# Kernel tuning notes

Hardware: AMD Instinct MI355X
Metric: run time of the kernel (lower is better)

## Reference

```python
import jax, jax.numpy as jnp
import numpy as np


def setup_inputs() -> dict:
    key = jax.random.key(0)
    ks = jax.random.split(key, 8)
    B, S, Nc, C, Cseed = 4, 4096, 8192, 512, 256
    return {
        "query_xyz": jax.random.normal(ks[0], (B, S, 3), dtype=jnp.float32),
        "ref_xyz": jax.random.normal(ks[1], (B, Nc, 3), dtype=jnp.float32),
        "ref_feat": jax.random.normal(ks[2], (B, C, Nc), dtype=jnp.float32),
        "seed_features": jax.random.normal(ks[3], (B, Cseed, S), dtype=jnp.float32),
        "W_seed_proj": jax.random.normal(ks[4], (Cseed, C), dtype=jnp.float32) * 0.02,
        "b_seed_proj": jax.random.normal(ks[5], (Cseed,), dtype=jnp.float32) * 0.02,
        "W_concat_proj": jax.random.normal(ks[6], (Cseed, 2 * Cseed), dtype=jnp.float32) * 0.02,
        "b_concat_proj": jax.random.normal(ks[7], (Cseed,), dtype=jnp.float32) * 0.02,
    }


def _nn_gather(query_xyz, ref_xyz, ref_feat):
    # torch.cdist(p=2) + argmin: argmin over squared distance is identical
    # (sqrt is monotonic), so we skip the sqrt.
    q2 = jnp.sum(query_xyz * query_xyz, axis=-1, keepdims=True)      # (B,S,1)
    r2 = jnp.sum(ref_xyz * ref_xyz, axis=-1)[:, None, :]             # (B,1,Nc)
    qr = jnp.einsum("bsd,bnd->bsn", query_xyz, ref_xyz)              # (B,S,Nc)
    d2 = q2 + r2 - 2.0 * qr                                          # (B,S,Nc)
    idx = jnp.argmin(d2, axis=-1)                                    # (B,S) int
    # gather nearest-neighbor features: (B,C,Nc) -> (B,C,S)
    return jnp.take_along_axis(ref_feat, idx[:, None, :], axis=2)


def reference(query_xyz, ref_xyz, ref_feat, seed_features,
              W_seed_proj, b_seed_proj, W_concat_proj, b_concat_proj):
    lift3d_raw = _nn_gather(query_xyz, ref_xyz, ref_feat)            # (B,C,S)
    # 1x1 Conv1d == channel matmul
    lift3d_seed = jnp.einsum("oc,bcs->bos", W_seed_proj, lift3d_raw) \
                  + b_seed_proj[None, :, None]                       # (B,256,S)
    fused = jnp.concatenate([seed_features, lift3d_seed], axis=1)    # (B,512,S)
    out = jnp.einsum("oc,bcs->bos", W_concat_proj, fused) \
          + b_concat_proj[None, :, None]                             # (B,256,S)
    return out
```

## Files before the change

kernel.cpp:

```cpp
#include <hip/hip_runtime.h>

#define B_   4
#define S_   4096
#define NC   8192
#define C_   512
#define CS   256
#define KTOT 768

typedef __attribute__((ext_vector_type(8))) short short8;
typedef __attribute__((ext_vector_type(4))) float f32x4;

static __device__ __forceinline__ unsigned short f2bf(float x) {
    unsigned u = __builtin_bit_cast(unsigned, x);
    unsigned r = u + 0x7FFFu + ((u >> 16) & 1u);
    return (unsigned short)(r >> 16);
}

__global__ __launch_bounds__(256) void prep_kernel(
        const float* __restrict__ rxyz, float4* __restrict__ refpk,
        const float* __restrict__ Wcat, const float* __restrict__ Wseed,
        unsigned short* __restrict__ Wcomb,
        const float* __restrict__ bseed, const float* __restrict__ bcat,
        float* __restrict__ beff,
        const float* __restrict__ seed, unsigned short* __restrict__ seedT) {
    __shared__ float sa[64][68];
    __shared__ float sbt[64][68];
    int bid = blockIdx.x;
    int tid = threadIdx.x;

    if (bid < 64) {
        int w = tid >> 6, l = tid & 63;
        int o = bid * 4 + w;
        float4 wv = *(const float4*)(Wcat + (size_t)o * 512 + 256 + l * 4);
        float4 bb = *(const float4*)(bseed + l * 4);
        float acc = __fmul_rn(wv.x, bb.x);
        acc = fmaf(wv.y, bb.y, acc);
        acc = fmaf(wv.z, bb.z, acc);
        acc = fmaf(wv.w, bb.w, acc);
        #pragma unroll
        for (int off = 32; off > 0; off >>= 1) acc += __shfl_down(acc, off);
        if (l == 0) beff[o] = acc + bcat[o];
    } else if (bid < 96) {
        int xb = bid - 64;
        int tc = (xb & 7) * 64;
        int to = (xb >> 3) * 64;
        int tx = tid & 15, ty = tid >> 4;
        float acc[4][4] = {};
        for (int kt = 0; kt < 256; kt += 64) {
            __syncthreads();
            #pragma unroll
            for (int r = 0; r < 4; ++r) {
                int oo = r * 16 + ty;
                float4 v = *(const float4*)(Wcat + (size_t)(to + oo) * 512 + 256 + kt + tx * 4);
                sa[oo][tx * 4 + 0] = v.x;
                sa[oo][tx * 4 + 1] = v.y;
                sa[oo][tx * 4 + 2] = v.z;
                sa[oo][tx * 4 + 3] = v.w;
                float4 u = *(const float4*)(Wseed + (size_t)(kt + oo) * 512 + tc + tx * 4);
                sbt[oo][tx * 4 + 0] = u.x;
                sbt[oo][tx * 4 + 1] = u.y;
                sbt[oo][tx * 4 + 2] = u.z;
                sbt[oo][tx * 4 + 3] = u.w;
            }
            __syncthreads();
            for (int k = 0; k < 64; ++k) {
                float a[4], bb2[4];
                #pragma unroll
                for (int i = 0; i < 4; ++i) a[i] = sa[ty * 4 + i][k];
                #pragma unroll
                for (int j = 0; j < 4; ++j) bb2[j] = sbt[k][tx * 4 + j];
                #pragma unroll
                for (int i = 0; i < 4; ++i)
                    #pragma unroll
                    for (int j = 0; j < 4; ++j)
                        acc[i][j] = fmaf(a[i], bb2[j], acc[i][j]);
            }
        }
        #pragma unroll
        for (int i = 0; i < 4; ++i)
            #pragma unroll
            for (int j = 0; j < 4; ++j)
                Wcomb[(size_t)(to + ty * 4 + i) * KTOT + 256 + tc + tx * 4 + j] = f2bf(acc[i][j]);
    } else if (bid < 160) {
        int g = ((bid - 96) * 256 + tid) * 4;
        int o = g >> 8, cc = g & 255;
        float4 v = *(const float4*)(Wcat + (size_t)o * 512 + cc);
        ushort4 ov;
        ov.x = f2bf(v.x); ov.y = f2bf(v.y); ov.z = f2bf(v.z); ov.w = f2bf(v.w);
        *(ushort4*)(Wcomb + (size_t)o * KTOT + cc) = ov;
    } else if (bid < 288) {
        int gid = (bid - 160) * 256 + tid;
        float x = rxyz[gid * 3 + 0];
        float y = rxyz[gid * 3 + 1];
        float z = rxyz[gid * 3 + 2];
        float r2 = __fadd_rn(__fadd_rn(__fmul_rn(x, x), __fmul_rn(y, y)), __fmul_rn(z, z));
        refpk[gid] = make_float4(x, y, z, r2);
    } else {
        int id = bid - 288;
        int b = id >> 8;
        int rem = id & 255;
        int c0 = (rem >> 6) * 64;
        int s0 = (rem & 63) * 64;
        int tx = tid & 15, ty = tid >> 4;
        #pragma unroll
        for (int r = 0; r < 4; ++r) {
            int cc = r * 16 + ty;
            float4 v = *(const float4*)(seed + ((size_t)b * CS + c0 + cc) * S_ + s0 + tx * 4);
            sa[tx * 4 + 0][cc] = v.x;
            sa[tx * 4 + 1][cc] = v.y;
            sa[tx * 4 + 2][cc] = v.z;
            sa[tx * 4 + 3][cc] = v.w;
        }
        __syncthreads();
        #pragma unroll
        for (int r = 0; r < 4; ++r) {
            int n = r * 16 + ty;
            ushort4 o;
            o.x = f2bf(sa[n][tx * 4 + 0]);
            o.y = f2bf(sa[n][tx * 4 + 1]);
            o.z = f2bf(sa[n][tx * 4 + 2]);
            o.w = f2bf(sa[n][tx * 4 + 3]);
            *(ushort4*)(seedT + ((size_t)b * S_ + s0 + n) * CS + c0 + tx * 4) = o;
        }
    }
}

__global__ __launch_bounds__(256, 4) void mid_kernel(
        const float* __restrict__ qxyz, const float4* __restrict__ refpk,
        float* __restrict__ pval, int* __restrict__ pidx,
        const float* __restrict__ rf, unsigned short* __restrict__ refT) {
    __shared__ float t[64][65];
    int bid = blockIdx.x;
    int tid = threadIdx.x;

    if (bid % 3 != 0) {
        int id = bid - bid / 3 - 1;
        int b = id >> 10;
        int c0 = ((id >> 7) & 7) * 64;
        int n0 = (id & 127) * 64;
        int tx = tid & 15, ty = tid >> 4;
        #pragma unroll
        for (int r = 0; r < 4; ++r) {
            int cc = r * 16 + ty;
            float4 v = *(const float4*)(rf + ((size_t)b * C_ + c0 + cc) * NC + n0 + tx * 4);
            t[tx * 4 + 0][cc] = v.x;
            t[tx * 4 + 1][cc] = v.y;
            t[tx * 4 + 2][cc] = v.z;
            t[tx * 4 + 3][cc] = v.w;
        }
        __syncthreads();
        #pragma unroll
        for (int r = 0; r < 4; ++r) {
            int n = r * 16 + ty;
            ushort4 o;
            o.x = f2bf(t[n][tx * 4 + 0]);
            o.y = f2bf(t[n][tx * 4 + 1]);
            o.z = f2bf(t[n][tx * 4 + 2]);
            o.w = f2bf(t[n][tx * 4 + 3]);
            *(ushort4*)(refT + ((size_t)b * NC + n0 + n) * C_ + c0 + tx * 4) = o;
        }
    } else {
        int aid = bid / 3;
        int sblk = aid & 127;
        int c = (aid >> 7) & 3;
        int b = aid >> 9;
        int lane = tid & 63;
        int qg = tid >> 6;
        int sbase = sblk * 32 + qg * 8;

        float qx[8], qy[8], qz[8], q2[8];
        #pragma unroll
        for (int q = 0; q < 8; ++q) {
            const float* qp = qxyz + ((size_t)(b * S_ + sbase + q)) * 3;
            qx[q] = qp[0]; qy[q] = qp[1]; qz[q] = qp[2];
            q2[q] = __fadd_rn(__fadd_rn(__fmul_rn(qx[q], qx[q]), __fmul_rn(qy[q], qy[q])),
                              __fmul_rn(qz[q], qz[q]));
        }

        const float4* ep = refpk + (size_t)b * NC + c * 2048 + lane;
        float best[8];
        int bj[8];
        #pragma unroll
        for (int q = 0; q < 8; ++q) { best[q] = 3.4028235e38f; bj[q] = 0; }

        float4 r0 = ep[0];
        float4 r1 = ep[64];
        #pragma unroll 2
        for (int j = 0; j < 32; j += 2) {
            float4 r2 = r0, r3 = r1;
            if (j + 2 < 32) {
                r2 = ep[(j + 2) * 64];
                r3 = ep[(j + 3) * 64];
            }
            #pragma unroll
            for (int q = 0; q < 8; ++q) {
                float qr = __fadd_rn(__fadd_rn(__fmul_rn(qx[q], r0.x), __fmul_rn(qy[q], r0.y)),
                                     __fmul_rn(qz[q], r0.z));
                float s = __fadd_rn(q2[q], r0.w);
                float d2 = fmaf(qr, -2.0f, s);
                if (d2 < best[q]) { best[q] = d2; bj[q] = j; }
            }
            #pragma unroll
            for (int q = 0; q < 8; ++q) {
                float qr = __fadd_rn(__fadd_rn(__fmul_rn(qx[q], r1.x), __fmul_rn(qy[q], r1.y)),
                                     __fmul_rn(qz[q], r1.z));
                float s = __fadd_rn(q2[q], r1.w);
                float d2 = fmaf(qr, -2.0f, s);
                if (d2 < best[q]) { best[q] = d2; bj[q] = j + 1; }
            }
            r0 = r2;
            r1 = r3;
        }

        int bx[8];
        #pragma unroll
        for (int q = 0; q < 8; ++q) bx[q] = c * 2048 + bj[q] * 64 + lane;

        #pragma unroll
        for (int m = 1; m < 64; m <<= 1) {
            #pragma unroll
            for (int q = 0; q < 8; ++q) {
                float vv = __shfl_xor(best[q], m, 64);
                int xx = __shfl_xor(bx[q], m, 64);
                if (vv < best[q] || (vv == best[q] && xx < bx[q])) {
                    best[q] = vv; bx[q] = xx;
                }
            }
        }
        if (lane == 0) {
            #pragma unroll
            for (int q = 0; q < 8; ++q) {
                int qs = b * S_ + sbase + q;
                pval[qs * 4 + c] = best[q];
                pidx[qs * 4 + c] = bx[q];
            }
        }
    }
}

__global__ __launch_bounds__(256) void fused_gemm_kernel(
        const unsigned short* __restrict__ Wcomb,
        const unsigned short* __restrict__ seedT,
        const unsigned short* __restrict__ refT,
        const float* __restrict__ pval,
        const int* __restrict__ pidx,
        const float* __restrict__ beff,
        float* __restrict__ out) {
    __shared__ __align__(16) unsigned short sA[64][72];
    __shared__ __align__(16) unsigned short sB[64][72];
    __shared__ int sIdx[64];
    __shared__ float sBias[64];

    int tid = threadIdx.x;
    int b = blockIdx.z;
    int m0 = blockIdx.y * 64;
    int s0 = blockIdx.x * 64;
    if (tid < 64) {
        int qs = b * S_ + s0 + tid;
        float v = pval[qs * 4 + 0];
        int x = pidx[qs * 4 + 0];
        #pragma unroll
        for (int c = 1; c < 4; ++c) {
            float vv = pval[qs * 4 + c];
            int xx = pidx[qs * 4 + c];
            if (vv < v || (vv == v && xx < x)) { v = vv; x = xx; }
        }
        sIdx[tid] = x & (NC - 1);
        sBias[tid] = beff[m0 + tid];
    }

    int lane = tid & 63;
    int w = tid >> 6;
    int wm = w >> 1;
    int wn = w & 1;
    int ln = lane & 15;
    int quad = lane >> 4;
    int q8 = quad * 8;

    int mm   = tid >> 2;
    int kk16 = (tid & 3) << 4;
    const unsigned short* Arow = Wcomb + (size_t)(m0 + mm) * KTOT + kk16;
    const unsigned short* Srow = seedT + ((size_t)b * S_ + s0 + mm) * CS + kk16;

    f32x4 acc[2][2];
    #pragma unroll
    for (int i = 0; i < 2; ++i)
        #pragma unroll
        for (int j = 0; j < 2; ++j)
            acc[i][j] = (f32x4){0.f, 0.f, 0.f, 0.f};

    for (int ks = 0; ks < 12; ++ks) {
        int k0 = ks * 64;
        __syncthreads();
        *(short8*)&sA[mm][kk16]     = *(const short8*)(Arow + k0);
        *(short8*)&sA[mm][kk16 + 8] = *(const short8*)(Arow + k0 + 8);
        const unsigned short* Brow =
            (k0 < 256) ? (Srow + k0)
                       : (refT + ((size_t)b * NC + sIdx[mm]) * C_ + (k0 - 256) + kk16);
        *(short8*)&sB[mm][kk16]     = *(const short8*)(Brow);
        *(short8*)&sB[mm][kk16 + 8] = *(const short8*)(Brow + 8);
        __syncthreads();
        #pragma unroll
        for (int kf = 0; kf < 2; ++kf) {
            short8 af[2], bfr[2];
            #pragma unroll
            for (int i = 0; i < 2; ++i)
                af[i] = *(const short8*)&sA[wm * 32 + i * 16 + ln][kf * 32 + q8];
            #pragma unroll
            for (int j = 0; j < 2; ++j)
                bfr[j] = *(const short8*)&sB[wn * 32 + j * 16 + ln][kf * 32 + q8];
            #pragma unroll
            for (int i = 0; i < 2; ++i)
                #pragma unroll
                for (int j = 0; j < 2; ++j)
                    acc[i][j] = __builtin_amdgcn_mfma_f32_16x16x32_bf16(af[i], bfr[j], acc[i][j], 0, 0, 0);
        }
    }

    #pragma unroll
    for (int i = 0; i < 2; ++i) {
        int mb = wm * 32 + i * 16 + quad * 4;
        #pragma unroll
        for (int j = 0; j < 2; ++j) {
            int col = s0 + wn * 32 + j * 16 + ln;
            #pragma unroll
            for (int r = 0; r < 4; ++r) {
                int m = mb + r;
                out[((size_t)b * CS + m0 + m) * S_ + col] = acc[i][j][r] + sBias[m];
            }
        }
    }
}

extern "C" void kernel_launch(void* const* d_in, const int* in_sizes, int n_in,
                              void* d_out, int out_size, void* d_ws, size_t ws_size,
                              hipStream_t stream) {
    const float* qxyz  = (const float*)d_in[0];
    const float* rxyz  = (const float*)d_in[1];
    const float* rfeat = (const float*)d_in[2];
    const float* seed  = (const float*)d_in[3];
    const float* Wseed = (const float*)d_in[4];
    const float* bseed = (const float*)d_in[5];
    const float* Wcat  = (const float*)d_in[6];
    const float* bcat  = (const float*)d_in[7];
    float* out = (float*)d_out;

    char* ws = (char*)d_ws;
    float* pval           = (float*)(ws);
    int* pidx             = (int*)(ws + 262144);
    float* beff           = (float*)(ws + 524288);
    float4* refpk         = (float4*)(ws + 528384);
    unsigned short* Wcomb = (unsigned short*)(ws + 1052672);
    unsigned short* refT  = (unsigned short*)(ws + 1445888);
    unsigned short* seedT = (unsigned short*)(ws + 35000320);

    hipLaunchKernelGGL(prep_kernel, dim3(1312), dim3(256), 0, stream,
                       rxyz, refpk, Wcat, Wseed, Wcomb, bseed, bcat, beff, seed, seedT);
    hipLaunchKernelGGL(mid_kernel, dim3(6144), dim3(256), 0, stream,
                       qxyz, refpk, pval, pidx, rfeat, refT);
    hipLaunchKernelGGL(fused_gemm_kernel, dim3(64, 4, 4), dim3(256), 0, stream,
                       Wcomb, seedT, refT, pval, pidx, beff, out);
}
```

Baseline: 183.3 us.

## Move seed transpose into mid kernel and double-buffer GEMM shared tiles

The seed-feature transpose and bf16 conversion move out of the prep kernel into the mid kernel, interleaved with the nearest-neighbour search and ref-feature transpose blocks in a 7-block pattern, so the prep kernel shrinks to 288 blocks. The goal is to run the bandwidth-bound transposes alongside the compute-bound search. The fused GEMM now double-buffers its shared-memory A/B tiles, prefetching the next k-slice into registers while MFMAs run on the current one, which drops one barrier per iteration. The cost is twice the LDS footprint per block and more live registers.

```diff
diff --git a/kernel.cpp b/kernel.cpp
--- a/kernel.cpp
+++ b/kernel.cpp
@@ -21,8 +21,7 @@
         const float* __restrict__ Wcat, const float* __restrict__ Wseed,
         unsigned short* __restrict__ Wcomb,
         const float* __restrict__ bseed, const float* __restrict__ bcat,
-        float* __restrict__ beff,
-        const float* __restrict__ seed, unsigned short* __restrict__ seedT) {
+        float* __restrict__ beff) {
     __shared__ float sa[64][68];
     __shared__ float sbt[64][68];
     int bid = blockIdx.x;
@@ -88,53 +87,105 @@
         ushort4 ov;
         ov.x = f2bf(v.x); ov.y = f2bf(v.y); ov.z = f2bf(v.z); ov.w = f2bf(v.w);
         *(ushort4*)(Wcomb + (size_t)o * KTOT + cc) = ov;
-    } else if (bid < 288) {
+    } else {
         int gid = (bid - 160) * 256 + tid;
         float x = rxyz[gid * 3 + 0];
         float y = rxyz[gid * 3 + 1];
         float z = rxyz[gid * 3 + 2];
         float r2 = __fadd_rn(__fadd_rn(__fmul_rn(x, x), __fmul_rn(y, y)), __fmul_rn(z, z));
         refpk[gid] = make_float4(x, y, z, r2);
-    } else {
-        int id = bid - 288;
-        int b = id >> 8;
-        int rem = id & 255;
-        int c0 = (rem >> 6) * 64;
-        int s0 = (rem & 63) * 64;
-        int tx = tid & 15, ty = tid >> 4;
-        #pragma unroll
-        for (int r = 0; r < 4; ++r) {
-            int cc = r * 16 + ty;
-            float4 v = *(const float4*)(seed + ((size_t)b * CS + c0 + cc) * S_ + s0 + tx * 4);
-            sa[tx * 4 + 0][cc] = v.x;
-            sa[tx * 4 + 1][cc] = v.y;
-            sa[tx * 4 + 2][cc] = v.z;
-            sa[tx * 4 + 3][cc] = v.w;
-        }
-        __syncthreads();
-        #pragma unroll
-        for (int r = 0; r < 4; ++r) {
-            int n = r * 16 + ty;
-            ushort4 o;
-            o.x = f2bf(sa[n][tx * 4 + 0]);
-            o.y = f2bf(sa[n][tx * 4 + 1]);
-            o.z = f2bf(sa[n][tx * 4 + 2]);
-            o.w = f2bf(sa[n][tx * 4 + 3]);
-            *(ushort4*)(seedT + ((size_t)b * S_ + s0 + n) * CS + c0 + tx * 4) = o;
-        }
     }
 }
 
 __global__ __launch_bounds__(256, 4) void mid_kernel(
         const float* __restrict__ qxyz, const float4* __restrict__ refpk,
         float* __restrict__ pval, int* __restrict__ pidx,
-        const float* __restrict__ rf, unsigned short* __restrict__ refT) {
+        const float* __restrict__ rf, unsigned short* __restrict__ refT,
+        const float* __restrict__ seed, unsigned short* __restrict__ seedT) {
     __shared__ float t[64][65];
     int bid = blockIdx.x;
     int tid = threadIdx.x;
-
-    if (bid % 3 != 0) {
-        int id = bid - bid / 3 - 1;
+    int r7 = bid % 7;
+    int g7 = bid / 7;
+
+    if (r7 == 0 || r7 == 4) {
+        int aid = g7 * 2 + (r7 == 4);
+        int sblk = aid & 127;
+        int c = (aid >> 7) & 3;
+        int b = aid >> 9;
+        int lane = tid & 63;
+        int qg = tid >> 6;
+        int sbase = sblk * 32 + qg * 8;
+
+        float qx[8], qy[8], qz[8], q2[8];
+        #pragma unroll
+        for (int q = 0; q < 8; ++q) {
+            const float* qp = qxyz + ((size_t)(b * S_ + sbase + q)) * 3;
+            qx[q] = qp[0]; qy[q] = qp[1]; qz[q] = qp[2];
+            q2[q] = __fadd_rn(__fadd_rn(__fmul_rn(qx[q], qx[q]), __fmul_rn(qy[q], qy[q])),
+                              __fmul_rn(qz[q], qz[q]));
+        }
+
+        const float4* ep = refpk + (size_t)b * NC + c * 2048 + lane;
+        float best[8];
+        int bj[8];
+        #pragma unroll
+        for (int q = 0; q < 8; ++q) { best[q] = 3.4028235e38f; bj[q] = 0; }
+
+        float4 r0 = ep[0];
+        float4 r1 = ep[64];
+        #pragma unroll 2
+        for (int j = 0; j < 32; j += 2) {
+            float4 r2 = r0, r3 = r1;
+            if (j + 2 < 32) {
+                r2 = ep[(j + 2) * 64];
+                r3 = ep[(j + 3) * 64];
+            }
+            #pragma unroll
+            for (int q = 0; q < 8; ++q) {
+                float qr = __fadd_rn(__fadd_rn(__fmul_rn(qx[q], r0.x), __fmul_rn(qy[q], r0.y)),
+                                     __fmul_rn(qz[q], r0.z));
+                float s = __fadd_rn(q2[q], r0.w);
+                float d2 = fmaf(qr, -2.0f, s);
+                if (d2 < best[q]) { best[q] = d2; bj[q] = j; }
+            }
+            #pragma unroll
+            for (int q = 0; q < 8; ++q) {
+                float qr = __fadd_rn(__fadd_rn(__fmul_rn(qx[q], r1.x), __fmul_rn(qy[q], r1.y)),
+                                     __fmul_rn(qz[q], r1.z));
+                float s = __fadd_rn(q2[q], r1.w);
+                float d2 = fmaf(qr, -2.0f, s);
+                if (d2 < best[q]) { best[q] = d2; bj[q] = j + 1; }
+            }
+            r0 = r2;
+            r1 = r3;
+        }
+
+        int bx[8];
+        #pragma unroll
+        for (int q = 0; q < 8; ++q) bx[q] = c * 2048 + bj[q] * 64 + lane;
+
+        #pragma unroll
+        for (int m = 1; m < 64; m <<= 1) {
+            #pragma unroll
+            for (int q = 0; q < 8; ++q) {
+                float vv = __shfl_xor(best[q], m, 64);
+                int xx = __shfl_xor(bx[q], m, 64);
+                if (vv < best[q] || (vv == best[q] && xx < bx[q])) {
+                    best[q] = vv; bx[q] = xx;
+                }
+            }
+        }
+        if (lane == 0) {
+            #pragma unroll
+            for (int q = 0; q < 8; ++q) {
+                int qs = b * S_ + sbase + q;
+                pval[qs * 4 + c] = best[q];
+                pidx[qs * 4 + c] = bx[q];
+            }
+        }
+    } else if (r7 != 6) {
+        int id = g7 * 4 + (r7 - 1 - (r7 > 4 ? 1 : 0));
         int b = id >> 10;
         int c0 = ((id >> 7) & 7) * 64;
         int n0 = (id & 127) * 64;
@@ -160,80 +211,31 @@
             *(ushort4*)(refT + ((size_t)b * NC + n0 + n) * C_ + c0 + tx * 4) = o;
         }
     } else {
-        int aid = bid / 3;
-        int sblk = aid & 127;
-        int c = (aid >> 7) & 3;
-        int b = aid >> 9;
-        int lane = tid & 63;
-        int qg = tid >> 6;
-        int sbase = sblk * 32 + qg * 8;
-
-        float qx[8], qy[8], qz[8], q2[8];
-        #pragma unroll
-        for (int q = 0; q < 8; ++q) {
-            const float* qp = qxyz + ((size_t)(b * S_ + sbase + q)) * 3;
-            qx[q] = qp[0]; qy[q] = qp[1]; qz[q] = qp[2];
-            q2[q] = __fadd_rn(__fadd_rn(__fmul_rn(qx[q], qx[q]), __fmul_rn(qy[q], qy[q])),
-                              __fmul_rn(qz[q], qz[q]));
-        }
-
-        const float4* ep = refpk + (size_t)b * NC + c * 2048 + lane;
-        float best[8];
-        int bj[8];
-        #pragma unroll
-        for (int q = 0; q < 8; ++q) { best[q] = 3.4028235e38f; bj[q] = 0; }
-
-        float4 r0 = ep[0];
-        float4 r1 = ep[64];
-        #pragma unroll 2
-        for (int j = 0; j < 32; j += 2) {
-            float4 r2 = r0, r3 = r1;
-            if (j + 2 < 32) {
-                r2 = ep[(j + 2) * 64];
-                r3 = ep[(j + 3) * 64];
-            }
-            #pragma unroll
-            for (int q = 0; q < 8; ++q) {
-                float qr = __fadd_rn(__fadd_rn(__fmul_rn(qx[q], r0.x), __fmul_rn(qy[q], r0.y)),
-                                     __fmul_rn(qz[q], r0.z));
-                float s = __fadd_rn(q2[q], r0.w);
-                float d2 = fmaf(qr, -2.0f, s);
-                if (d2 < best[q]) { best[q] = d2; bj[q] = j; }
-            }
-            #pragma unroll
-            for (int q = 0; q < 8; ++q) {
-                float qr = __fadd_rn(__fadd_rn(__fmul_rn(qx[q], r1.x), __fmul_rn(qy[q], r1.y)),
-                                     __fmul_rn(qz[q], r1.z));
-                float s = __fadd_rn(q2[q], r1.w);
-                float d2 = fmaf(qr, -2.0f, s);
-                if (d2 < best[q]) { best[q] = d2; bj[q] = j + 1; }
-            }
-            r0 = r2;
-            r1 = r3;
-        }
-
-        int bx[8];
-        #pragma unroll
-        for (int q = 0; q < 8; ++q) bx[q] = c * 2048 + bj[q] * 64 + lane;
-
-        #pragma unroll
-        for (int m = 1; m < 64; m <<= 1) {
-            #pragma unroll
-            for (int q = 0; q < 8; ++q) {
-                float vv = __shfl_xor(best[q], m, 64);
-                int xx = __shfl_xor(bx[q], m, 64);
-                if (vv < best[q] || (vv == best[q] && xx < bx[q])) {
-                    best[q] = vv; bx[q] = xx;
-                }
-            }
-        }
-        if (lane == 0) {
-            #pragma unroll
-            for (int q = 0; q < 8; ++q) {
-                int qs = b * S_ + sbase + q;
-                pval[qs * 4 + c] = best[q];
-                pidx[qs * 4 + c] = bx[q];
-            }
+        int id = g7;
+        int b = id >> 8;
+        int rem = id & 255;
+        int c0 = (rem >> 6) * 64;
+        int s0 = (rem & 63) * 64;
+        int tx = tid & 15, ty = tid >> 4;
+        #pragma unroll
+        for (int r = 0; r < 4; ++r) {
+            int cc = r * 16 + ty;
+            float4 v = *(const float4*)(seed + ((size_t)b * CS + c0 + cc) * S_ + s0 + tx * 4);
+            t[tx * 4 + 0][cc] = v.x;
+            t[tx * 4 + 1][cc] = v.y;
+            t[tx * 4 + 2][cc] = v.z;
+            t[tx * 4 + 3][cc] = v.w;
+        }
+        __syncthreads();
+        #pragma unroll
+        for (int r = 0; r < 4; ++r) {
+            int n = r * 16 + ty;
+            ushort4 o;
+            o.x = f2bf(t[n][tx * 4 + 0]);
+            o.y = f2bf(t[n][tx * 4 + 1]);
+            o.z = f2bf(t[n][tx * 4 + 2]);
+            o.w = f2bf(t[n][tx * 4 + 3]);
+            *(ushort4*)(seedT + ((size_t)b * S_ + s0 + n) * CS + c0 + tx * 4) = o;
         }
     }
 }
@@ -246,8 +248,8 @@
         const int* __restrict__ pidx,
         const float* __restrict__ beff,
         float* __restrict__ out) {
-    __shared__ __align__(16) unsigned short sA[64][72];
-    __shared__ __align__(16) unsigned short sB[64][72];
+    __shared__ __align__(16) unsigned short sA[2][64][72];
+    __shared__ __align__(16) unsigned short sB[2][64][72];
     __shared__ int sIdx[64];
     __shared__ float sBias[64];
 
@@ -289,33 +291,57 @@
         for (int j = 0; j < 2; ++j)
             acc[i][j] = (f32x4){0.f, 0.f, 0.f, 0.f};
 
+    short8 ra0, ra1, rb0, rb1;
+
+    #define SLOAD(PK) do {                                                         \
+        int pk0 = (PK) * 64;                                                       \
+        ra0 = *(const short8*)(Arow + pk0);                                        \
+        ra1 = *(const short8*)(Arow + pk0 + 8);                                    \
+        const unsigned short* Brow =                                               \
+            (pk0 < 256) ? (Srow + pk0)                                             \
+                        : (refT + ((size_t)b * NC + sIdx[mm]) * C_                 \
+                           + (pk0 - 256) + kk16);                                  \
+        rb0 = *(const short8*)(Brow);                                              \
+        rb1 = *(const short8*)(Brow + 8);                                          \
+    } while (0)
+
+    #define SWRITE(BUF) do {                                                       \
+        *(short8*)&sA[BUF][mm][kk16]     = ra0;                                    \
+        *(short8*)&sA[BUF][mm][kk16 + 8] = ra1;                                    \
+        *(short8*)&sB[BUF][mm][kk16]     = rb0;                                    \
+        *(short8*)&sB[BUF][mm][kk16 + 8] = rb1;                                    \
+    } while (0)
+
+    SLOAD(0);
+    SWRITE(0);
+    __syncthreads();
+
+    int cur = 0;
     for (int ks = 0; ks < 12; ++ks) {
-        int k0 = ks * 64;
-        __syncthreads();
-        *(short8*)&sA[mm][kk16]     = *(const short8*)(Arow + k0);
-        *(short8*)&sA[mm][kk16 + 8] = *(const short8*)(Arow + k0 + 8);
-        const unsigned short* Brow =
-            (k0 < 256) ? (Srow + k0)
-                       : (refT + ((size_t)b * NC + sIdx[mm]) * C_ + (k0 - 256) + kk16);
-        *(short8*)&sB[mm][kk16]     = *(const short8*)(Brow);
-        *(short8*)&sB[mm][kk16 + 8] = *(const short8*)(Brow + 8);
-        __syncthreads();
+        if (ks < 11) SLOAD(ks + 1);
         #pragma unroll
         for (int kf = 0; kf < 2; ++kf) {
             short8 af[2], bfr[2];
             #pragma unroll
             for (int i = 0; i < 2; ++i)
-                af[i] = *(const short8*)&sA[wm * 32 + i * 16 + ln][kf * 32 + q8];
+                af[i] = *(const short8*)&sA[cur][wm * 32 + i * 16 + ln][kf * 32 + q8];
             #pragma unroll
             for (int j = 0; j < 2; ++j)
-                bfr[j] = *(const short8*)&sB[wn * 32 + j * 16 + ln][kf * 32 + q8];
+                bfr[j] = *(const short8*)&sB[cur][wn * 32 + j * 16 + ln][kf * 32 + q8];
             #pragma unroll
             for (int i = 0; i < 2; ++i)
                 #pragma unroll
                 for (int j = 0; j < 2; ++j)
                     acc[i][j] = __builtin_amdgcn_mfma_f32_16x16x32_bf16(af[i], bfr[j], acc[i][j], 0, 0, 0);
         }
-    }
+        if (ks < 11) {
+            SWRITE(cur ^ 1);
+            __syncthreads();
+            cur ^= 1;
+        }
+    }
+    #undef SLOAD
+    #undef SWRITE
 
     #pragma unroll
     for (int i = 0; i < 2; ++i) {
@@ -354,10 +380,10 @@
     unsigned short* refT  = (unsigned short*)(ws + 1445888);
     unsigned short* seedT = (unsigned short*)(ws + 35000320);
 
-    hipLaunchKernelGGL(prep_kernel, dim3(1312), dim3(256), 0, stream,
-                       rxyz, refpk, Wcat, Wseed, Wcomb, bseed, bcat, beff, seed, seedT);
-    hipLaunchKernelGGL(mid_kernel, dim3(6144), dim3(256), 0, stream,
-                       qxyz, refpk, pval, pidx, rfeat, refT);
+    hipLaunchKernelGGL(prep_kernel, dim3(288), dim3(256), 0, stream,
+                       rxyz, refpk, Wcat, Wseed, Wcomb, bseed, bcat, beff);
+    hipLaunchKernelGGL(mid_kernel, dim3(7168), dim3(256), 0, stream,
+                       qxyz, refpk, pval, pidx, rfeat, refT, seed, seedT);
     hipLaunchKernelGGL(fused_gemm_kernel, dim3(64, 4, 4), dim3(256), 0, stream,
                        Wcomb, seedT, refT, pval, pidx, beff, out);
 }
```

New measurement: 181.9 us. No clear change (-0.8%).
